# Kernel tuning notes

Hardware: AMD Instinct MI355X
Metric: run time of the kernel (lower is better)

The kernel has to match this reference:

```python
import jax, jax.numpy as jnp
import numpy as np

INPUT_DIM = 1024
HIDDEN_DIM = 128
TEMPERATURE = 1.0
TOPK = 10  # hard-coded k in the original forward


def setup_inputs() -> dict:
    key = jax.random.key(0)
    ks = jax.random.split(key, 7)
    B, N = 8, 50000
    s_in = 1.0 / np.sqrt(INPUT_DIM)
    s_h = 1.0 / np.sqrt(HIDDEN_DIM)
    return {
        "x": jax.random.normal(ks[0], (B, N, INPUT_DIM), dtype=jnp.float32),
        # torch Linear weight is [out,in]; we store transposed [in,out] for x @ W
        "Wv": jax.random.uniform(ks[1], (INPUT_DIM, HIDDEN_DIM), jnp.float32, -s_in, s_in),
        "bv": jax.random.uniform(ks[2], (HIDDEN_DIM,), jnp.float32, -s_in, s_in),
        "Wu": jax.random.uniform(ks[3], (INPUT_DIM, HIDDEN_DIM), jnp.float32, -s_in, s_in),
        "bu": jax.random.uniform(ks[4], (HIDDEN_DIM,), jnp.float32, -s_in, s_in),
        "Ww": jax.random.uniform(ks[5], (HIDDEN_DIM, 1), jnp.float32, -s_h, s_h),
        "bw": jax.random.uniform(ks[6], (1,), jnp.float32, -s_h, s_h),
    }


def reference(x, Wv, bv, Wu, bu, Ww, bw):
    # x: [B, N, D]. Dropout is identity in eval mode.
    def per_bag(xi):  # xi: [N, D]
        A_V = jnp.tanh(xi @ Wv + bv)              # [N, H]
        A_U = jax.nn.sigmoid(xi @ Wu + bu)        # [N, H] (gated attention)
        A = A_V * A_U
        scores = ((A @ Ww) + bw)[:, 0] / TEMPERATURE  # [N]
        _, top_idx = jax.lax.top_k(scores, TOPK)
        _, tail_idx = jax.lax.top_k(-scores, TOPK)
        idx = jnp.concatenate([top_idx, tail_idx])     # [2k]
        w = jax.nn.softmax(scores[idx])                # softmax over truncated set
        Z = w @ xi[idx]                                # [D]
        # dense analogue of the per-instance attention list (None -> 0)
        atten = jnp.zeros_like(scores).at[idx].set(w)  # [N]
        return Z, atten

    Z, atten = jax.vmap(per_bag)(x)  # Z: [B, D], atten: [B, N]
    return Z, atten
```

## Files before the change

kernel.cpp:

```cpp
#include <hip/hip_runtime.h>
#include <math.h>
#include <float.h>

#define INPUT_DIM 1024
#define HIDDEN 128
#define KSEL 10
#define KC 12

#define BM 64
#define BK 64
#define KT (INPUT_DIM / BK)
#define STH 256
#define NSEL1 32

typedef short short8 __attribute__((ext_vector_type(8)));
typedef float f32x4 __attribute__((ext_vector_type(4)));

static __device__ __forceinline__ unsigned short f2bf(float f) {
    union { float f; unsigned u; } v; v.f = f;
    unsigned r = v.u + 0x7FFF + ((v.u >> 16) & 1);
    return (unsigned short)(r >> 16);
}
static __device__ __forceinline__ float fast_tanh(float a) {
    float e = __expf(2.0f * a);
    return 1.0f - 2.0f / (e + 1.0f);
}
static __device__ __forceinline__ float fast_sigmoid(float a) {
    return 1.0f / (1.0f + __expf(-a));
}

__global__ __launch_bounds__(64) void repack_kernel(
    const float* __restrict__ Wv, const float* __restrict__ Wu,
    unsigned short* __restrict__ wp_hi)
{
    int bid = blockIdx.x;
    int l = threadIdx.x;
    int pc = (bid & 15) * 16 + (l & 15);
    int h = pc >> 1;
    const float* src = (pc & 1) ? Wu : Wv;
    int kbase = (bid >> 4) * 32 + (l >> 4) * 8;
    size_t off = ((size_t)bid * 64 + l) * 8;
    #pragma unroll
    for (int e = 0; e < 8; ++e)
        wp_hi[off + e] = f2bf(src[(size_t)(kbase + e) * HIDDEN + h]);
}

__global__ __launch_bounds__(STH) void scores_kernel(
    const float* __restrict__ x, const unsigned short* __restrict__ wp,
    const float* __restrict__ bv, const float* __restrict__ bu,
    const float* __restrict__ Ww, const float* __restrict__ bw,
    float* __restrict__ scores, float* __restrict__ atten, int N)
{
    __shared__ __align__(16) unsigned short xs[4][BM * BK];
    __shared__ float partial[4][BM];

    const int tid = threadIdx.x;
    const int l = tid & 63;
    const int w = tid >> 6;
    const int b = blockIdx.y;
    const int i0 = blockIdx.x * BM;
    const float* xb = x + (size_t)b * N * INPUT_DIM;

    const float* gp0 = xb + (size_t)min(i0 + w * 16 + (l >> 3), N - 1) * INPUT_DIM + (l & 7) * 8;
    const float* gp1 = xb + (size_t)min(i0 + w * 16 + 8 + (l >> 3), N - 1) * INPUT_DIM + (l & 7) * 8;
    const int xw0 = (w * 16 + (l >> 3)) * BK + (((l & 7) ^ (l >> 3)) * 8);
    const int xw1 = (w * 16 + 8 + (l >> 3)) * BK + (((l & 7) ^ (l >> 3)) * 8);

    f32x4 acc[4][4];
    #pragma unroll
    for (int m = 0; m < 4; ++m)
        #pragma unroll
        for (int n = 0; n < 4; ++n)
            acc[m][n] = (f32x4){0.f, 0.f, 0.f, 0.f};

#define XLOAD(X0, X1, X2, X3, T) do { \
        const size_t _o = (size_t)min((T), KT - 1) * BK; \
        X0 = *(const float4*)(gp0 + _o); \
        X1 = *(const float4*)(gp0 + _o + 4); \
        X2 = *(const float4*)(gp1 + _o); \
        X3 = *(const float4*)(gp1 + _o + 4); \
    } while (0)

#define XWRITE(X0, X1, X2, X3, SLOT) do { \
        unsigned p0, p1, p2, p3, q0, q1, q2, q3; \
        asm("v_cvt_pk_bf16_f32 %0, %1, %2" : "=v"(p0) : "v"(X0.x), "v"(X0.y)); \
        asm("v_cvt_pk_bf16_f32 %0, %1, %2" : "=v"(p1) : "v"(X0.z), "v"(X0.w)); \
        asm("v_cvt_pk_bf16_f32 %0, %1, %2" : "=v"(p2) : "v"(X1.x), "v"(X1.y)); \
        asm("v_cvt_pk_bf16_f32 %0, %1, %2" : "=v"(p3) : "v"(X1.z), "v"(X1.w)); \
        asm("v_cvt_pk_bf16_f32 %0, %1, %2" : "=v"(q0) : "v"(X2.x), "v"(X2.y)); \
        asm("v_cvt_pk_bf16_f32 %0, %1, %2" : "=v"(q1) : "v"(X2.z), "v"(X2.w)); \
        asm("v_cvt_pk_bf16_f32 %0, %1, %2" : "=v"(q2) : "v"(X3.x), "v"(X3.y)); \
        asm("v_cvt_pk_bf16_f32 %0, %1, %2" : "=v"(q3) : "v"(X3.z), "v"(X3.w)); \
        *(uint4*)(&xs[(SLOT)][xw0]) = make_uint4(p0, p1, p2, p3); \
        *(uint4*)(&xs[(SLOT)][xw1]) = make_uint4(q0, q1, q2, q3); \
    } while (0)

#define BLOAD(KT_) do { \
        _Pragma("unroll") \
        for (int ks = 0; ks < 2; ++ks) \
            _Pragma("unroll") \
            for (int n = 0; n < 4; ++n) { \
                unsigned boff = (unsigned)(((((KT_) * 2 + ks) * 16 + w * 4 + n) * 64 + l) * 8); \
                bh[ks][n] = *(const short8*)(wp + boff); \
            } \
    } while (0)

#define MFMA_KT(SLOT) do { \
        __builtin_amdgcn_s_setprio(1); \
        _Pragma("unroll") \
        for (int ks = 0; ks < 2; ++ks) \
            _Pragma("unroll") \
            for (int m = 0; m < 4; ++m) { \
                int rowt = m * 16 + (l & 15); \
                int chunk = (ks * 4 + (l >> 4)) ^ (l & 7); \
                short8 a = *(const short8*)(&xs[(SLOT)][rowt * BK + chunk * 8]); \
                _Pragma("unroll") \
                for (int n = 0; n < 4; ++n) \
                    acc[m][n] = __builtin_amdgcn_mfma_f32_16x16x32_bf16(a, bh[ks][n], acc[m][n], 0, 0, 0); \
            } \
        __builtin_amdgcn_s_setprio(0); \
    } while (0)

#define LGKM_BARRIER() do { \
        asm volatile("s_waitcnt lgkmcnt(0)" ::: "memory"); \
        __builtin_amdgcn_s_barrier(); \
    } while (0)

    short8 bh[2][4];
    float4 a0, a1, a2, a3, c0, c1, c2, c3;

    XLOAD(a0, a1, a2, a3, 0);
    XWRITE(a0, a1, a2, a3, 0);
    XLOAD(a0, a1, a2, a3, 1);
    XLOAD(c0, c1, c2, c3, 2);
    LGKM_BARRIER();

    for (int j = 0; j < KT / 4; ++j) {
        #pragma unroll
        for (int ii = 0; ii < 4; ++ii) {
            const int kt = j * 4 + ii;
            BLOAD(kt);
            MFMA_KT(ii);
            __builtin_amdgcn_sched_barrier(0);
            if ((ii & 1) == 0) {
                XWRITE(a0, a1, a2, a3, (ii + 1) & 3);
                XLOAD(a0, a1, a2, a3, kt + 3);
            } else {
                XWRITE(c0, c1, c2, c3, (ii + 1) & 3);
                XLOAD(c0, c1, c2, c3, kt + 3);
            }
            __builtin_amdgcn_sched_barrier(0);
            LGKM_BARRIER();
        }
    }

#undef XLOAD
#undef XWRITE
#undef BLOAD
#undef MFMA_KT
#undef LGKM_BARRIER

    float bvv[4], buu[4], www[4];
    #pragma unroll
    for (int n = 0; n < 4; ++n) {
        int h = (w * 64 + n * 16 + (l & 15)) >> 1;
        bvv[n] = bv[h]; buu[n] = bu[h]; www[n] = Ww[h];
    }
    const bool isV = ((l & 1) == 0);

    #pragma unroll
    for (int m = 0; m < 4; ++m) {
        float cs[4] = {0.f, 0.f, 0.f, 0.f};
        #pragma unroll
        for (int n = 0; n < 4; ++n) {
            #pragma unroll
            for (int r = 0; r < 4; ++r) {
                float v = acc[m][n][r];
                float u = __shfl_xor(v, 1, 64);
                if (isV)
                    cs[r] += fast_tanh(v + bvv[n]) * fast_sigmoid(u + buu[n]) * www[n];
            }
        }
        #pragma unroll
        for (int r = 0; r < 4; ++r) {
            #pragma unroll
            for (int off = 1; off < 16; off <<= 1)
                cs[r] += __shfl_xor(cs[r], off, 64);
        }
        if ((l & 15) == 0) {
            #pragma unroll
            for (int r = 0; r < 4; ++r)
                partial[w][m * 16 + (l >> 4) * 4 + r] = cs[r];
        }
    }
    __syncthreads();

    if (tid < BM) {
        int gi2 = i0 + tid;
        if (gi2 < N) {
            float s = bw[0] + partial[0][tid] + partial[1][tid]
                            + partial[2][tid] + partial[3][tid];
            scores[(size_t)b * N + gi2] = s;
            atten[(size_t)b * N + gi2] = 0.0f;
        }
    }
}

__global__ __launch_bounds__(64) void select1_kernel(
    const float* __restrict__ scores, float* __restrict__ cv, int* __restrict__ ci,
    int N, int CH)
{
    const int r = blockIdx.x, b = blockIdx.y;
    const int tid = threadIdx.x;
    const float* s = scores + (size_t)b * N;
    const int start = r * CH;
    const int end = min(N, start + CH);

    float tv[KC]; int ti[KC];
    float lv[KC]; int li[KC];
    #pragma unroll
    for (int j = 0; j < KC; ++j) { tv[j] = -FLT_MAX; ti[j] = -1; lv[j] = FLT_MAX; li[j] = -1; }

    for (int i = start + tid; i < end; i += 64) {
        float v = s[i];
        if (v > tv[KC-1]) {
            #pragma unroll
            for (int j = KC-1; j >= 1; --j) {
                if (v > tv[j-1])      { tv[j] = tv[j-1]; ti[j] = ti[j-1]; }
                else if (v > tv[j])   { tv[j] = v;       ti[j] = i;       }
            }
            if (v > tv[0]) { tv[0] = v; ti[0] = i; }
        }
        if (v < lv[KC-1]) {
            #pragma unroll
            for (int j = KC-1; j >= 1; --j) {
                if (v < lv[j-1])      { lv[j] = lv[j-1]; li[j] = li[j-1]; }
                else if (v < lv[j])   { lv[j] = v;       li[j] = i;       }
            }
            if (v < lv[0]) { lv[0] = v; li[0] = i; }
        }
    }

    size_t base = ((size_t)b * NSEL1 + r) * 2 * KC;
    for (int rd = 0; rd < KC; ++rd) {
        float v = tv[0]; int who = tid;
        #pragma unroll
        for (int off = 32; off > 0; off >>= 1) {
            float ov = __shfl_down(v, off, 64);
            int ow = __shfl_down(who, off, 64);
            if (ov > v) { v = ov; who = ow; }
        }
        int bwho = __shfl(who, 0, 64);
        if (tid == bwho) {
            cv[base + rd] = tv[0]; ci[base + rd] = ti[0];
            #pragma unroll
            for (int j = 0; j < KC-1; ++j) { tv[j] = tv[j+1]; ti[j] = ti[j+1]; }
            tv[KC-1] = -FLT_MAX;
        }
    }
    for (int rd = 0; rd < KC; ++rd) {
        float v = lv[0]; int who = tid;
        #pragma unroll
        for (int off = 32; off > 0; off >>= 1) {
            float ov = __shfl_down(v, off, 64);
            int ow = __shfl_down(who, off, 64);
            if (ov < v) { v = ov; who = ow; }
        }
        int bwho = __shfl(who, 0, 64);
        if (tid == bwho) {
            cv[base + KC + rd] = lv[0]; ci[base + KC + rd] = li[0];
            #pragma unroll
            for (int j = 0; j < KC-1; ++j) { lv[j] = lv[j+1]; li[j] = li[j+1]; }
            lv[KC-1] = FLT_MAX;
        }
    }
}

__global__ __launch_bounds__(64) void select2_kernel(
    const float* __restrict__ cv, const int* __restrict__ ci,
    int* __restrict__ cand_idx)
{
    const int b = blockIdx.x;
    const int tid = threadIdx.x;

    float tv[KC]; int ti[KC];
    float lv[KC]; int li[KC];
    #pragma unroll
    for (int j = 0; j < KC; ++j) { tv[j] = -FLT_MAX; ti[j] = -1; lv[j] = FLT_MAX; li[j] = -1; }

    for (int c = tid; c < NSEL1 * KC; c += 64) {
        int rr = c / KC, jj = c % KC;
        size_t base = ((size_t)b * NSEL1 + rr) * 2 * KC;
        {
            float v = cv[base + jj]; int idx = ci[base + jj];
            if (v > tv[KC-1]) {
                #pragma unroll
                for (int j = KC-1; j >= 1; --j) {
                    if (v > tv[j-1])      { tv[j] = tv[j-1]; ti[j] = ti[j-1]; }
                    else if (v > tv[j])   { tv[j] = v;       ti[j] = idx;     }
                }
                if (v > tv[0]) { tv[0] = v; ti[0] = idx; }
            }
        }
        {
            float v = cv[base + KC + jj]; int idx = ci[base + KC + jj];
            if (v < lv[KC-1]) {
                #pragma unroll
                for (int j = KC-1; j >= 1; --j) {
                    if (v < lv[j-1])      { lv[j] = lv[j-1]; li[j] = li[j-1]; }
                    else if (v < lv[j])   { lv[j] = v;       li[j] = idx;     }
                }
                if (v < lv[0]) { lv[0] = v; li[0] = idx; }
            }
        }
    }

    for (int rd = 0; rd < KC; ++rd) {
        float v = tv[0]; int who = tid;
        #pragma unroll
        for (int off = 32; off > 0; off >>= 1) {
            float ov = __shfl_down(v, off, 64);
            int ow = __shfl_down(who, off, 64);
            if (ov > v) { v = ov; who = ow; }
        }
        int bwho = __shfl(who, 0, 64);
        if (tid == bwho) {
            cand_idx[b * 2 * KC + rd] = ti[0];
            #pragma unroll
            for (int j = 0; j < KC-1; ++j) { tv[j] = tv[j+1]; ti[j] = ti[j+1]; }
            tv[KC-1] = -FLT_MAX;
        }
    }
    for (int rd = 0; rd < KC; ++rd) {
        float v = lv[0]; int who = tid;
        #pragma unroll
        for (int off = 32; off > 0; off >>= 1) {
            float ov = __shfl_down(v, off, 64);
            int ow = __shfl_down(who, off, 64);
            if (ov < v) { v = ov; who = ow; }
        }
        int bwho = __shfl(who, 0, 64);
        if (tid == bwho) {
            cand_idx[b * 2 * KC + KC + rd] = li[0];
            #pragma unroll
            for (int j = 0; j < KC-1; ++j) { lv[j] = lv[j+1]; li[j] = li[j+1]; }
            lv[KC-1] = FLT_MAX;
        }
    }
}

__global__ __launch_bounds__(256) void rescore_kernel(
    const float* __restrict__ x,
    const float* __restrict__ Wv, const float* __restrict__ bv,
    const float* __restrict__ Wu, const float* __restrict__ bu,
    const float* __restrict__ Ww, const float* __restrict__ bw,
    const int* __restrict__ cand_idx, float* __restrict__ cand_score, int N)
{
    const int j = blockIdx.x, b = blockIdx.y;
    const int tid = threadIdx.x;
    __shared__ float xsr[INPUT_DIM];
    __shared__ float sp[4];

    int idx = cand_idx[b * 2 * KC + j];
    const float* xr = x + ((size_t)b * N + idx) * INPUT_DIM;
    *(float4*)(&xsr[tid * 4]) = *(const float4*)(&xr[tid * 4]);
    __syncthreads();

    const int h = tid >> 1;
    const int isU = tid & 1;
    const float* W = isU ? Wu : Wv;
    float s = 0.f;
    #pragma unroll 8
    for (int k = 0; k < INPUT_DIM; ++k)
        s = fmaf(xsr[k], W[(size_t)k * HIDDEN + h], s);

    float other = __shfl_xor(s, 1, 64);
    float g = 0.f;
    if (!isU) {
        float vv = tanhf(s + bv[h]);
        float uu = 1.0f / (1.0f + expf(-(other + bu[h])));
        g = vv * uu * Ww[h];
    }
    #pragma unroll
    for (int off = 1; off < 64; off <<= 1) g += __shfl_xor(g, off, 64);
    if ((tid & 63) == 0) sp[tid >> 6] = g;
    __syncthreads();
    if (tid == 0)
        cand_score[b * 2 * KC + j] = sp[0] + sp[1] + sp[2] + sp[3] + bw[0];
}

__global__ __launch_bounds__(256) void final_kernel(
    const float* __restrict__ x, const int* __restrict__ cand_idx,
    const float* __restrict__ cand_score,
    float* __restrict__ atten, float* __restrict__ Z, int N)
{
    const int b = blockIdx.x;
    const int tid = threadIdx.x;
    __shared__ int fidx[2 * KSEL];
    __shared__ float fw[2 * KSEL];

    if (tid == 0) {
        float cs[2 * KC]; int ciX[2 * KC]; bool used[2 * KC];
        #pragma unroll
        for (int j2 = 0; j2 < 2 * KC; ++j2) {
            cs[j2] = cand_score[b * 2 * KC + j2];
            ciX[j2] = cand_idx[b * 2 * KC + j2];
            used[j2] = false;
        }
        float fs[2 * KSEL];
        for (int r = 0; r < KSEL; ++r) {
            int best = -1; float bvv = -FLT_MAX;
            for (int j2 = 0; j2 < KC; ++j2)
                if (!used[j2] && cs[j2] > bvv) { bvv = cs[j2]; best = j2; }
            used[best] = true; fidx[r] = ciX[best]; fs[r] = bvv;
        }
        for (int r = 0; r < KSEL; ++r) {
            int best = -1; float bvv = FLT_MAX;
            for (int j2 = KC; j2 < 2 * KC; ++j2)
                if (!used[j2] && cs[j2] < bvv) { bvv = cs[j2]; best = j2; }
            used[best] = true; fidx[KSEL + r] = ciX[best]; fs[KSEL + r] = bvv;
        }
        float m = -FLT_MAX;
        for (int j2 = 0; j2 < 2 * KSEL; ++j2) m = fmaxf(m, fs[j2]);
        float e[2 * KSEL], sum = 0.f;
        for (int j2 = 0; j2 < 2 * KSEL; ++j2) { e[j2] = expf(fs[j2] - m); sum += e[j2]; }
        float inv = 1.0f / sum;
        for (int j2 = 0; j2 < 2 * KSEL; ++j2) {
            fw[j2] = e[j2] * inv;
            atten[(size_t)b * N + fidx[j2]] = fw[j2];
        }
    }
    __syncthreads();

    float4 acc = make_float4(0.f, 0.f, 0.f, 0.f);
    #pragma unroll
    for (int j2 = 0; j2 < 2 * KSEL; ++j2) {
        int idx = fidx[j2];
        float wgt = fw[j2];
        const float4* xr = (const float4*)(x + ((size_t)b * N + idx) * INPUT_DIM);
        float4 v = xr[tid];
        acc.x = fmaf(wgt, v.x, acc.x);
        acc.y = fmaf(wgt, v.y, acc.y);
        acc.z = fmaf(wgt, v.z, acc.z);
        acc.w = fmaf(wgt, v.w, acc.w);
    }
    ((float4*)(Z + (size_t)b * INPUT_DIM))[tid] = acc;
}

extern "C" void kernel_launch(void* const* d_in, const int* in_sizes, int n_in,
                              void* d_out, int out_size, void* d_ws, size_t ws_size,
                              hipStream_t stream)
{
    const float* x  = (const float*)d_in[0];
    const float* Wv = (const float*)d_in[1];
    const float* bv = (const float*)d_in[2];
    const float* Wu = (const float*)d_in[3];
    const float* bu = (const float*)d_in[4];
    const float* Ww = (const float*)d_in[5];
    const float* bw = (const float*)d_in[6];

    const int B = 8;
    const int N = in_sizes[0] / (B * INPUT_DIM);

    float* Z = (float*)d_out;
    float* atten = (float*)d_out + (size_t)B * INPUT_DIM;

    char* p = (char*)d_ws;
    float* scores = (float*)p;                  p += (size_t)B * N * sizeof(float);
    unsigned short* wp = (unsigned short*)p;    p += (size_t)INPUT_DIM * 256 * sizeof(unsigned short);
    float* cand_v = (float*)p;                  p += (size_t)B * NSEL1 * 2 * KC * sizeof(float);
    int* cand_i = (int*)p;                      p += (size_t)B * NSEL1 * 2 * KC * sizeof(int);
    int* cand_idx = (int*)p;                    p += (size_t)B * 2 * KC * sizeof(int);
    float* cand_score = (float*)p;

    repack_kernel<<<512, 64, 0, stream>>>(Wv, Wu, wp);

    dim3 g1((N + BM - 1) / BM, B);
    scores_kernel<<<g1, STH, 0, stream>>>(x, wp, bv, bu, Ww, bw, scores, atten, N);

    int CH = (N + NSEL1 - 1) / NSEL1;
    dim3 g2(NSEL1, B);
    select1_kernel<<<g2, 64, 0, stream>>>(scores, cand_v, cand_i, N, CH);
    select2_kernel<<<B, 64, 0, stream>>>(cand_v, cand_i, cand_idx);

    dim3 g3(2 * KC, B);
    rescore_kernel<<<g3, 256, 0, stream>>>(x, Wv, bv, Wu, bu, Ww, bw, cand_idx, cand_score, N);
    final_kernel<<<B, 256, 0, stream>>>(x, cand_idx, cand_score, atten, Z, N);
}
```

Baseline: 549.6 us.

## Use single-wave 16-row blocks computing all hidden columns without barriers

The scores GEMM moves from 256-thread blocks over 64 rows to 64-thread single-wave blocks over 16 rows. Each wave now computes all 256 packed V/U columns, with a two-slot LDS buffer and the B fragments loaded from global memory in groups interleaved with the MFMAs. Because each block is a single wave, the block barriers and the cross-wave partial-sum reduction in shared memory go away. In exchange, every wave streams the whole packed weight matrix, which is four times more weight traffic per row than before. The extra cache pressure could outweigh what the barrier removal saves.

```diff
diff --git a/kernel.cpp b/kernel.cpp
--- a/kernel.cpp
+++ b/kernel.cpp
@@ -7,10 +7,9 @@
 #define KSEL 10
 #define KC 12
 
-#define BM 64
+#define WROWS 16
 #define BK 64
 #define KT (INPUT_DIM / BK)
-#define STH 256
 #define NSEL1 32
 
 typedef short short8 __attribute__((ext_vector_type(8)));
@@ -45,163 +44,141 @@
         wp_hi[off + e] = f2bf(src[(size_t)(kbase + e) * HIDDEN + h]);
 }
 
-__global__ __launch_bounds__(STH) void scores_kernel(
+__global__ __launch_bounds__(64) void scores_kernel(
     const float* __restrict__ x, const unsigned short* __restrict__ wp,
     const float* __restrict__ bv, const float* __restrict__ bu,
     const float* __restrict__ Ww, const float* __restrict__ bw,
     float* __restrict__ scores, float* __restrict__ atten, int N)
 {
-    __shared__ __align__(16) unsigned short xs[4][BM * BK];
-    __shared__ float partial[4][BM];
-
-    const int tid = threadIdx.x;
-    const int l = tid & 63;
-    const int w = tid >> 6;
+    __shared__ __align__(16) unsigned short xs[2][WROWS * BK];
+
+    const int l = threadIdx.x;
     const int b = blockIdx.y;
-    const int i0 = blockIdx.x * BM;
+    const int i0 = blockIdx.x * WROWS;
     const float* xb = x + (size_t)b * N * INPUT_DIM;
 
-    const float* gp0 = xb + (size_t)min(i0 + w * 16 + (l >> 3), N - 1) * INPUT_DIM + (l & 7) * 8;
-    const float* gp1 = xb + (size_t)min(i0 + w * 16 + 8 + (l >> 3), N - 1) * INPUT_DIM + (l & 7) * 8;
-    const int xw0 = (w * 16 + (l >> 3)) * BK + (((l & 7) ^ (l >> 3)) * 8);
-    const int xw1 = (w * 16 + 8 + (l >> 3)) * BK + (((l & 7) ^ (l >> 3)) * 8);
-
-    f32x4 acc[4][4];
-    #pragma unroll
-    for (int m = 0; m < 4; ++m)
-        #pragma unroll
-        for (int n = 0; n < 4; ++n)
-            acc[m][n] = (f32x4){0.f, 0.f, 0.f, 0.f};
-
-#define XLOAD(X0, X1, X2, X3, T) do { \
-        const size_t _o = (size_t)min((T), KT - 1) * BK; \
-        X0 = *(const float4*)(gp0 + _o); \
-        X1 = *(const float4*)(gp0 + _o + 4); \
-        X2 = *(const float4*)(gp1 + _o); \
-        X3 = *(const float4*)(gp1 + _o + 4); \
+    const int srow = l >> 2;
+    const float* gp = xb + (size_t)min(i0 + srow, N - 1) * INPUT_DIM + (l & 3) * 16;
+    const int wb0 = srow * BK + (((2 * (l & 3))     ^ (srow & 7)) * 8);
+    const int wb1 = srow * BK + (((2 * (l & 3) + 1) ^ (srow & 7)) * 8);
+
+    f32x4 acc[16];
+    #pragma unroll
+    for (int n = 0; n < 16; ++n) acc[n] = (f32x4){0.f, 0.f, 0.f, 0.f};
+
+    float4 xa[4], xc[4];
+    short8 q0[4], q1[4];
+
+#define XLOAD(X, T) do { \
+        const float* _p = gp + (size_t)min((T), KT - 1) * BK; \
+        X[0] = *(const float4*)(_p); \
+        X[1] = *(const float4*)(_p + 4); \
+        X[2] = *(const float4*)(_p + 8); \
+        X[3] = *(const float4*)(_p + 12); \
     } while (0)
 
-#define XWRITE(X0, X1, X2, X3, SLOT) do { \
-        unsigned p0, p1, p2, p3, q0, q1, q2, q3; \
-        asm("v_cvt_pk_bf16_f32 %0, %1, %2" : "=v"(p0) : "v"(X0.x), "v"(X0.y)); \
-        asm("v_cvt_pk_bf16_f32 %0, %1, %2" : "=v"(p1) : "v"(X0.z), "v"(X0.w)); \
-        asm("v_cvt_pk_bf16_f32 %0, %1, %2" : "=v"(p2) : "v"(X1.x), "v"(X1.y)); \
-        asm("v_cvt_pk_bf16_f32 %0, %1, %2" : "=v"(p3) : "v"(X1.z), "v"(X1.w)); \
-        asm("v_cvt_pk_bf16_f32 %0, %1, %2" : "=v"(q0) : "v"(X2.x), "v"(X2.y)); \
-        asm("v_cvt_pk_bf16_f32 %0, %1, %2" : "=v"(q1) : "v"(X2.z), "v"(X2.w)); \
-        asm("v_cvt_pk_bf16_f32 %0, %1, %2" : "=v"(q2) : "v"(X3.x), "v"(X3.y)); \
-        asm("v_cvt_pk_bf16_f32 %0, %1, %2" : "=v"(q3) : "v"(X3.z), "v"(X3.w)); \
-        *(uint4*)(&xs[(SLOT)][xw0]) = make_uint4(p0, p1, p2, p3); \
-        *(uint4*)(&xs[(SLOT)][xw1]) = make_uint4(q0, q1, q2, q3); \
+#define XWRITE(X, SLOT) do { \
+        unsigned u0, u1, u2, u3, u4, u5, u6, u7; \
+        asm("v_cvt_pk_bf16_f32 %0, %1, %2" : "=v"(u0) : "v"(X[0].x), "v"(X[0].y)); \
+        asm("v_cvt_pk_bf16_f32 %0, %1, %2" : "=v"(u1) : "v"(X[0].z), "v"(X[0].w)); \
+        asm("v_cvt_pk_bf16_f32 %0, %1, %2" : "=v"(u2) : "v"(X[1].x), "v"(X[1].y)); \
+        asm("v_cvt_pk_bf16_f32 %0, %1, %2" : "=v"(u3) : "v"(X[1].z), "v"(X[1].w)); \
+        asm("v_cvt_pk_bf16_f32 %0, %1, %2" : "=v"(u4) : "v"(X[2].x), "v"(X[2].y)); \
+        asm("v_cvt_pk_bf16_f32 %0, %1, %2" : "=v"(u5) : "v"(X[2].z), "v"(X[2].w)); \
+        asm("v_cvt_pk_bf16_f32 %0, %1, %2" : "=v"(u6) : "v"(X[3].x), "v"(X[3].y)); \
+        asm("v_cvt_pk_bf16_f32 %0, %1, %2" : "=v"(u7) : "v"(X[3].z), "v"(X[3].w)); \
+        *(uint4*)(&xs[(SLOT)][wb0]) = make_uint4(u0, u1, u2, u3); \
+        *(uint4*)(&xs[(SLOT)][wb1]) = make_uint4(u4, u5, u6, u7); \
     } while (0)
 
-#define BLOAD(KT_) do { \
+#define AREAD(DST, SLOT, KS) \
+        DST = *(const short8*)(&xs[(SLOT)][(l & 15) * BK + ((((KS) * 4 + (l >> 4)) ^ (l & 7)) * 8)])
+
+#define BLOADG(Q, KT_, G) do { \
+        const unsigned _kg = (unsigned)((KT_) * 2 + ((G) >> 2)); \
+        const unsigned _nb = ((G) & 3) * 4; \
         _Pragma("unroll") \
-        for (int ks = 0; ks < 2; ++ks) \
-            _Pragma("unroll") \
-            for (int n = 0; n < 4; ++n) { \
-                unsigned boff = (unsigned)(((((KT_) * 2 + ks) * 16 + w * 4 + n) * 64 + l) * 8); \
-                bh[ks][n] = *(const short8*)(wp + boff); \
-            } \
+        for (int j = 0; j < 4; ++j) \
+            Q[j] = *(const short8*)(wp + (((_kg * 16 + _nb + j) * 64 + l) * 8)); \
     } while (0)
 
-#define MFMA_KT(SLOT) do { \
+#define MFMAG(Q, A, G) do { \
+        const int _nb = ((G) & 3) * 4; \
+        _Pragma("unroll") \
+        for (int j = 0; j < 4; ++j) \
+            acc[_nb + j] = __builtin_amdgcn_mfma_f32_16x16x32_bf16(A, Q[j], acc[_nb + j], 0, 0, 0); \
+    } while (0)
+
+#define BODY(KT_, XSET) do { \
+        const int _slot = (KT_) & 1; \
+        short8 a0, a1; \
+        AREAD(a0, _slot, 0); \
+        AREAD(a1, _slot, 1); \
+        XWRITE(XSET, _slot ^ 1);           \
+        asm volatile("" ::: "memory"); \
         __builtin_amdgcn_s_setprio(1); \
-        _Pragma("unroll") \
-        for (int ks = 0; ks < 2; ++ks) \
-            _Pragma("unroll") \
-            for (int m = 0; m < 4; ++m) { \
-                int rowt = m * 16 + (l & 15); \
-                int chunk = (ks * 4 + (l >> 4)) ^ (l & 7); \
-                short8 a = *(const short8*)(&xs[(SLOT)][rowt * BK + chunk * 8]); \
-                _Pragma("unroll") \
-                for (int n = 0; n < 4; ++n) \
-                    acc[m][n] = __builtin_amdgcn_mfma_f32_16x16x32_bf16(a, bh[ks][n], acc[m][n], 0, 0, 0); \
-            } \
+        BLOADG(q0, KT_, 0); \
+        BLOADG(q1, KT_, 1); MFMAG(q0, a0, 0); \
+        BLOADG(q0, KT_, 2); MFMAG(q1, a0, 1); \
+        BLOADG(q1, KT_, 3); MFMAG(q0, a0, 2); \
+        BLOADG(q0, KT_, 4); MFMAG(q1, a0, 3); \
+        BLOADG(q1, KT_, 5); MFMAG(q0, a1, 4); \
+        BLOADG(q0, KT_, 6); MFMAG(q1, a1, 5); \
+        BLOADG(q1, KT_, 7); MFMAG(q0, a1, 6); \
+        MFMAG(q1, a1, 7); \
         __builtin_amdgcn_s_setprio(0); \
+        __builtin_amdgcn_sched_barrier(0); \
+        XLOAD(XSET, (KT_) + 3);            \
+        asm volatile("" ::: "memory"); \
     } while (0)
 
-#define LGKM_BARRIER() do { \
-        asm volatile("s_waitcnt lgkmcnt(0)" ::: "memory"); \
-        __builtin_amdgcn_s_barrier(); \
-    } while (0)
-
-    short8 bh[2][4];
-    float4 a0, a1, a2, a3, c0, c1, c2, c3;
-
-    XLOAD(a0, a1, a2, a3, 0);
-    XWRITE(a0, a1, a2, a3, 0);
-    XLOAD(a0, a1, a2, a3, 1);
-    XLOAD(c0, c1, c2, c3, 2);
-    LGKM_BARRIER();
-
-    for (int j = 0; j < KT / 4; ++j) {
-        #pragma unroll
-        for (int ii = 0; ii < 4; ++ii) {
-            const int kt = j * 4 + ii;
-            BLOAD(kt);
-            MFMA_KT(ii);
-            __builtin_amdgcn_sched_barrier(0);
-            if ((ii & 1) == 0) {
-                XWRITE(a0, a1, a2, a3, (ii + 1) & 3);
-                XLOAD(a0, a1, a2, a3, kt + 3);
-            } else {
-                XWRITE(c0, c1, c2, c3, (ii + 1) & 3);
-                XLOAD(c0, c1, c2, c3, kt + 3);
-            }
-            __builtin_amdgcn_sched_barrier(0);
-            LGKM_BARRIER();
-        }
+    XLOAD(xa, 0);
+    XWRITE(xa, 0);
+    XLOAD(xa, 1);
+    XLOAD(xc, 2);
+    asm volatile("" ::: "memory");
+
+    for (int kt2 = 0; kt2 < KT / 2; ++kt2) {
+        BODY(2 * kt2,     xa);
+        BODY(2 * kt2 + 1, xc);
     }
 
 #undef XLOAD
 #undef XWRITE
-#undef BLOAD
-#undef MFMA_KT
-#undef LGKM_BARRIER
-
-    float bvv[4], buu[4], www[4];
-    #pragma unroll
-    for (int n = 0; n < 4; ++n) {
-        int h = (w * 64 + n * 16 + (l & 15)) >> 1;
-        bvv[n] = bv[h]; buu[n] = bu[h]; www[n] = Ww[h];
-    }
+#undef AREAD
+#undef BLOADG
+#undef MFMAG
+#undef BODY
+
     const bool isV = ((l & 1) == 0);
-
-    #pragma unroll
-    for (int m = 0; m < 4; ++m) {
-        float cs[4] = {0.f, 0.f, 0.f, 0.f};
-        #pragma unroll
-        for (int n = 0; n < 4; ++n) {
-            #pragma unroll
-            for (int r = 0; r < 4; ++r) {
-                float v = acc[m][n][r];
-                float u = __shfl_xor(v, 1, 64);
-                if (isV)
-                    cs[r] += fast_tanh(v + bvv[n]) * fast_sigmoid(u + buu[n]) * www[n];
+    float cs[4] = {0.f, 0.f, 0.f, 0.f};
+    #pragma unroll
+    for (int n = 0; n < 16; ++n) {
+        int h = (n * 16 + (l & 15)) >> 1;
+        float bvv = bv[h], buu = bu[h], www = Ww[h];
+        #pragma unroll
+        for (int r = 0; r < 4; ++r) {
+            float v = acc[n][r];
+            float u = __shfl_xor(v, 1, 64);
+            if (isV)
+                cs[r] += fast_tanh(v + bvv) * fast_sigmoid(u + buu) * www;
+        }
+    }
+    #pragma unroll
+    for (int r = 0; r < 4; ++r)
+        #pragma unroll
+        for (int off = 1; off < 16; off <<= 1)
+            cs[r] += __shfl_xor(cs[r], off, 64);
+
+    if ((l & 15) == 0) {
+        float bw0 = bw[0];
+        #pragma unroll
+        for (int r = 0; r < 4; ++r) {
+            int gi = i0 + (l >> 4) * 4 + r;
+            if (gi < N) {
+                scores[(size_t)b * N + gi] = cs[r] + bw0;
+                atten[(size_t)b * N + gi] = 0.0f;
             }
-        }
-        #pragma unroll
-        for (int r = 0; r < 4; ++r) {
-            #pragma unroll
-            for (int off = 1; off < 16; off <<= 1)
-                cs[r] += __shfl_xor(cs[r], off, 64);
-        }
-        if ((l & 15) == 0) {
-            #pragma unroll
-            for (int r = 0; r < 4; ++r)
-                partial[w][m * 16 + (l >> 4) * 4 + r] = cs[r];
-        }
-    }
-    __syncthreads();
-
-    if (tid < BM) {
-        int gi2 = i0 + tid;
-        if (gi2 < N) {
-            float s = bw[0] + partial[0][tid] + partial[1][tid]
-                            + partial[2][tid] + partial[3][tid];
-            scores[(size_t)b * N + gi2] = s;
-            atten[(size_t)b * N + gi2] = 0.0f;
         }
     }
 }
@@ -475,8 +452,8 @@
 
     repack_kernel<<<512, 64, 0, stream>>>(Wv, Wu, wp);
 
-    dim3 g1((N + BM - 1) / BM, B);
-    scores_kernel<<<g1, STH, 0, stream>>>(x, wp, bv, bu, Ww, bw, scores, atten, N);
+    dim3 g1((N + WROWS - 1) / WROWS, B);
+    scores_kernel<<<g1, 64, 0, stream>>>(x, wp, bv, bu, Ww, bw, scores, atten, N);
 
     int CH = (N + NSEL1 - 1) / NSEL1;
     dim3 g2(NSEL1, B);
```

New measurement: 1.011 ms. +84.0%, slower.
